# Optimization experiments

Measured on AMD Instinct MI355X. Metric: run time of the kernel, lower is better.

Reference implementation:

```python
import jax, jax.numpy as jnp
import numpy as np

N = 100000   # nodes
E = 300000   # directed edges (avg degree 3, molecular graphs)
G = 4000     # molecules in the batch
IN = 9
HID = 128
HEADS = 4
NEG_SLOPE = 0.2


def setup_inputs() -> dict:
    key = jax.random.key(0)
    ks = jax.random.split(key, 12)
    x = jax.random.normal(ks[0], (N, IN), dtype=jnp.float32)
    edge_index = jax.random.randint(ks[1], (2, E), 0, N, dtype=jnp.int32)
    batch = jnp.sort(jax.random.randint(ks[2], (N,), 0, G, dtype=jnp.int32))
    s = 0.1  # keep activations in a sane range
    W1 = jax.random.normal(ks[3], (IN, HEADS * HID), dtype=jnp.float32) * s
    a_src1 = jax.random.normal(ks[4], (HEADS, HID), dtype=jnp.float32) * s
    a_dst1 = jax.random.normal(ks[5], (HEADS, HID), dtype=jnp.float32) * s
    b1 = jax.random.normal(ks[6], (HEADS * HID,), dtype=jnp.float32) * s
    W2 = jax.random.normal(ks[7], (HEADS * HID, HID), dtype=jnp.float32) * s
    a_src2 = jax.random.normal(ks[8], (1, HID), dtype=jnp.float32) * s
    a_dst2 = jax.random.normal(ks[9], (1, HID), dtype=jnp.float32) * s
    b2 = jax.random.normal(ks[10], (HID,), dtype=jnp.float32) * s
    return {"x": x, "edge_index": edge_index, "batch": batch,
            "W1": W1, "a_src1": a_src1, "a_dst1": a_dst1, "b1": b1,
            "W2": W2, "a_src2": a_src2, "a_dst2": a_dst2, "b2": b2}


def _gat_conv(x, edge_index, W, a_src, a_dst, b, heads, out_ch, concat):
    """PyG GATConv: linear proj, per-edge leaky-relu attention logits,
    segment softmax over destination nodes, scatter-add aggregation.
    add_self_loops=True (PyG default)."""
    n = x.shape[0]
    loops = jnp.arange(n, dtype=edge_index.dtype)
    src = jnp.concatenate([edge_index[0], loops])
    dst = jnp.concatenate([edge_index[1], loops])

    h = (x @ W).reshape(n, heads, out_ch)                  # [N, H, C]
    alpha_s = jnp.einsum('nhc,hc->nh', h, a_src)           # [N, H]
    alpha_d = jnp.einsum('nhc,hc->nh', h, a_dst)           # [N, H]

    logits = jax.nn.leaky_relu(alpha_s[src] + alpha_d[dst], NEG_SLOPE)  # [Etot, H]
    # numerically stable segment softmax over incoming edges of each dst
    m = jax.ops.segment_max(logits, dst, num_segments=n)   # [N, H] (finite: self-loops)
    e = jnp.exp(logits - m[dst])
    z = jax.ops.segment_sum(e, dst, num_segments=n)
    alpha = e / (z[dst] + 1e-16)                           # [Etot, H]

    msg = h[src] * alpha[:, :, None]                       # [Etot, H, C]
    out = jax.ops.segment_sum(msg, dst, num_segments=n)    # [N, H, C]
    if concat:
        out = out.reshape(n, heads * out_ch)
    else:
        out = out.mean(axis=1)
    return out + b


def reference(x, edge_index, batch, W1, a_src1, a_dst1, b1, W2, a_src2, a_dst2, b2):
    h = jax.nn.elu(_gat_conv(x, edge_index, W1, a_src1, a_dst1, b1, HEADS, HID, True))
    h = jax.nn.elu(_gat_conv(h, edge_index, W2, a_src2, a_dst2, b2, 1, HID, True))
    # global mean pool per graph
    sums = jax.ops.segment_sum(h, batch, num_segments=G)   # [G, HID]
    cnt = jax.ops.segment_sum(jnp.ones((h.shape[0],), h.dtype), batch, num_segments=G)
    return sums / jnp.maximum(cnt, 1.0)[:, None]
```

## Files before the change

### kernel.cpp

```cpp
#include <hip/hip_runtime.h>

#define N_NODES 100000
#define N_EDGES 300000
#define N_GRAPHS 4000
#define CAP 32

typedef float f32x4 __attribute__((ext_vector_type(4)));
typedef __bf16 bf16x8 __attribute__((ext_vector_type(8)));
typedef __bf16 bf16x2 __attribute__((ext_vector_type(2)));

static const size_t OFF_XA    = 0;
static const size_t OFF_AD4   = OFF_XA + (size_t)N_NODES * 16;
static const size_t OFF_AGG   = OFF_AD4 + (size_t)N_NODES * 4;
static const size_t OFF_P2B   = OFF_AGG + (size_t)N_NODES * 36;
static const size_t OFF_ASAD2 = OFF_P2B + (size_t)N_NODES * 64;
static const size_t OFF_WSB   = OFF_ASAD2 + (size_t)N_NODES * 2;
static const size_t OFF_INVC  = OFF_WSB + 32768;
static const size_t OFF_INT   = OFF_INVC + 4096;

#define PRE_NODE_END 391
#define PRE_PACKB_END 455
#define PRE_DEG_END 846
#define PRE_OUT_END 1346
#define PRE_INV_END 1362

__device__ __forceinline__ float lrelu(float x) { return x < 0.f ? 0.2f * x : x; }
__device__ __forceinline__ float elu(float x)   { return x > 0.f ? x : __expf(x) - 1.f; }

__global__ __launch_bounds__(256) void k_pre(
    const float* __restrict__ x, const float* __restrict__ W1,
    const float* __restrict__ a_src1, const float* __restrict__ a_dst1,
    const float* __restrict__ W2, const int* __restrict__ batch,
    float* __restrict__ xa, float* __restrict__ ad4,
    __bf16* __restrict__ wsB, int* __restrict__ deg, float* __restrict__ out,
    float* __restrict__ inv_cnt) {
    int b = blockIdx.x, tid = threadIdx.x;
    if (b < PRE_NODE_END) {
        __shared__ float wf[72];
        if (tid < 72) {
            int isd = tid / 36, r = tid % 36, k = r / 4, h = r % 4;
            const float* a = isd ? a_dst1 : a_src1;
            float s = 0.f;
            for (int c = 0; c < 128; c++) s += W1[k * 512 + h * 128 + c] * a[h * 128 + c];
            wf[tid] = s;
        }
        __syncthreads();
        int n = b * 256 + tid;
        if (n >= N_NODES) return;
        float xv[9];
#pragma unroll
        for (int k = 0; k < 9; k++) xv[k] = x[n * 9 + k];
        float as[4], ad[4];
#pragma unroll
        for (int h = 0; h < 4; h++) {
            float s = 0.f, d = 0.f;
#pragma unroll
            for (int k = 0; k < 9; k++) {
                s += xv[k] * wf[k * 4 + h];
                d += xv[k] * wf[36 + k * 4 + h];
            }
            as[h] = s; ad[h] = d;
        }
        f32x4* xp = (f32x4*)(xa + (size_t)n * 16);
        xp[0] = (f32x4){xv[0], xv[1], xv[2], xv[3]};
        xp[1] = (f32x4){xv[4], xv[5], xv[6], xv[7]};
        xp[2] = (f32x4){xv[8], as[0], as[1], as[2]};
        xp[3] = (f32x4){as[3], 0.f, 0.f, 0.f};
        *(f32x4*)(ad4 + (size_t)n * 4) = (f32x4){ad[0], ad[1], ad[2], ad[3]};
    } else if (b < PRE_PACKB_END) {
        int t = (b - PRE_NODE_END) * 256 + tid;
#pragma unroll
        for (int m = 0; m < 4; m++) {
            int idx = t * 4 + m;
            int k = idx >> 7, nn = idx & 127;
            wsB[(size_t)nn * 512 + k] = (__bf16)W2[(size_t)k * 128 + nn];
        }
    } else if (b < PRE_DEG_END) {
        int idx = (b - PRE_PACKB_END) * 256 + tid;
        if (idx < N_NODES) deg[idx] = 0;
    } else if (b < PRE_OUT_END) {
        int idx = (b - PRE_DEG_END) * 256 + tid;
        if (idx < 128000) ((f32x4*)out)[idx] = (f32x4){0.f, 0.f, 0.f, 0.f};
    } else {
        int g = (b - PRE_OUT_END) * 256 + tid;
        if (g >= N_GRAPHS) return;
        int lo = 0, hi = N_NODES;
        while (lo < hi) { int mid = (lo + hi) >> 1; if (batch[mid] < g) lo = mid + 1; else hi = mid; }
        int s = lo; hi = N_NODES;
        while (lo < hi) { int mid = (lo + hi) >> 1; if (batch[mid] < g + 1) lo = mid + 1; else hi = mid; }
        int c = lo - s;
        inv_cnt[g] = 1.f / (float)(c > 0 ? c : 1);
    }
}

__global__ void k_bucket(const int* __restrict__ ei, int* __restrict__ deg,
                         int* __restrict__ bucket) {
    int e = blockIdx.x * 256 + threadIdx.x;
    if (e >= N_EDGES) return;
    int s = ei[e], d = ei[N_EDGES + e];
    int slot = atomicAdd(&deg[d], 1);
    if (slot < CAP) bucket[d * CAP + slot] = s;
}

__global__ void k_agg(const float* __restrict__ xa, const float* __restrict__ ad4,
                      const int* __restrict__ deg, const int* __restrict__ bucket,
                      __bf16* __restrict__ agg) {
    int t = blockIdx.x * 256 + threadIdx.x;
    int n = t >> 2, h = t & 3;
    if (n >= N_NODES) return;
    float ad = ad4[(size_t)n * 4 + h];
    int dg = deg[n];
    if (dg > CAP) dg = CAP;
    float acc[9] = {};
    float z = 0.f;
    {
        const f32x4* xp = (const f32x4*)(xa + (size_t)n * 16);
        f32x4 v0 = xp[0], v1 = xp[1], v2 = xp[2], v3 = xp[3];
        float asl = (h == 0) ? v2.y : (h == 1) ? v2.z : (h == 2) ? v2.w : v3.x;
        float e = __expf(lrelu(asl + ad));
        z += e;
        acc[0] += e * v0.x; acc[1] += e * v0.y; acc[2] += e * v0.z; acc[3] += e * v0.w;
        acc[4] += e * v1.x; acc[5] += e * v1.y; acc[6] += e * v1.z; acc[7] += e * v1.w;
        acc[8] += e * v2.x;
    }
    for (int j = 0; j < dg; j++) {
        int src = bucket[n * CAP + j];
        const f32x4* xp = (const f32x4*)(xa + (size_t)src * 16);
        f32x4 v0 = xp[0], v1 = xp[1], v2 = xp[2], v3 = xp[3];
        float asl = (h == 0) ? v2.y : (h == 1) ? v2.z : (h == 2) ? v2.w : v3.x;
        float e = __expf(lrelu(asl + ad));
        z += e;
        acc[0] += e * v0.x; acc[1] += e * v0.y; acc[2] += e * v0.z; acc[3] += e * v0.w;
        acc[4] += e * v1.x; acc[5] += e * v1.y; acc[6] += e * v1.z; acc[7] += e * v1.w;
        acc[8] += e * v2.x;
    }
    float inv = 1.f / z;
    bf16x8 p0;
#pragma unroll
    for (int k = 0; k < 8; k++) p0[k] = (__bf16)(acc[k] * inv);
    __bf16* dst = agg + (size_t)n * 72 + h * 16;
    *(bf16x8*)dst = p0;
    dst[8] = (__bf16)(acc[8] * inv);
}

__global__ __launch_bounds__(512, 4) void k_gemm(
    const __bf16* __restrict__ agg, const float* __restrict__ W1,
    const float* __restrict__ b1, const __bf16* __restrict__ wsB,
    const float* __restrict__ a_src2, const float* __restrict__ a_dst2,
    __bf16* __restrict__ p2b, float* __restrict__ asad2) {
    __shared__ __bf16 As[64 * 512];
    __shared__ __bf16 AgT[64 * 72];
    __shared__ float red2[64 * 16];
    const int tid = threadIdx.x;
    const int lane = tid & 63;
    const int w = tid >> 6;
    const int i = lane & 15;
    const int q = lane >> 4;
    const int m0 = blockIdx.x * 64;

    bf16x8 breg[16];
    {
        const __bf16* bp = wsB + (size_t)(w * 16 + i) * 512 + q * 8;
#pragma unroll
        for (int kc = 0; kc < 16; kc++) breg[kc] = *(const bf16x8*)(bp + kc * 32);
    }

    for (int idx = tid; idx < 576; idx += 512) {
        int row = idx / 9, c8 = idx - row * 9;
        int gr = m0 + row;
        bf16x8 v;
        if (gr < N_NODES) v = *(const bf16x8*)(agg + (size_t)gr * 72 + c8 * 8);
        else {
#pragma unroll
            for (int k = 0; k < 8; k++) v[k] = (__bf16)0.f;
        }
        *(bf16x8*)&AgT[row * 72 + c8 * 8] = v;
    }
    __syncthreads();

    {
        int row = tid & 63;
        int kg = __builtin_amdgcn_readfirstlane(tid >> 6);
        int h = kg >> 1;
        float ag[9];
        {
            bf16x8 a8 = *(const bf16x8*)&AgT[row * 72 + h * 16];
#pragma unroll
            for (int k = 0; k < 8; k++) ag[k] = (float)a8[k];
            ag[8] = (float)AgT[row * 72 + h * 16 + 8];
        }
        int rt = row >> 4, il = row & 15;
#pragma unroll
        for (int c8 = 0; c8 < 8; c8++) {
            int j0 = kg * 64 + c8 * 8;
            float o[8];
#pragma unroll
            for (int e = 0; e < 8; e++) o[e] = b1[j0 + e];
#pragma unroll
            for (int k = 0; k < 9; k++) {
                const float* wp = &W1[k * 512 + j0];
#pragma unroll
                for (int e = 0; e < 8; e++) o[e] += ag[k] * wp[e];
            }
            bf16x8 pk;
#pragma unroll
            for (int e = 0; e < 8; e++) pk[e] = (__bf16)elu(o[e]);
            int tile = rt * 16 + (kg * 2 + (c8 >> 2));
            *(bf16x8*)&As[tile * 512 + ((c8 & 3) * 16 + il) * 8] = pk;
        }
    }
    __syncthreads();

    f32x4 acc[4];
#pragma unroll
    for (int r = 0; r < 4; r++) acc[r] = (f32x4){0.f, 0.f, 0.f, 0.f};
#pragma unroll
    for (int kc = 0; kc < 16; kc++) {
#pragma unroll
        for (int rt = 0; rt < 4; rt++) {
            bf16x8 af = *(const bf16x8*)&As[(rt * 16 + kc) * 512 + lane * 8];
            acc[rt] = __builtin_amdgcn_mfma_f32_16x16x32_bf16(af, breg[kc], acc[rt], 0, 0, 0);
        }
    }

    float as2 = a_src2[w * 16 + i];
    float ad2 = a_dst2[w * 16 + i];
#pragma unroll
    for (int rt = 0; rt < 4; rt++) {
#pragma unroll
        for (int qq = 0; qq < 4; qq++) {
            int row = rt * 16 + q * 4 + qq;
            float v = acc[rt][qq];
            if (m0 + row < N_NODES)
                p2b[(size_t)(m0 + row) * 128 + w * 16 + i] = (__bf16)v;
            float s = v * as2, d = v * ad2;
#pragma unroll
            for (int off = 1; off < 16; off <<= 1) {
                s += __shfl_xor(s, off);
                d += __shfl_xor(d, off);
            }
            if (i == 0) {
                red2[row * 16 + w * 2] = s;
                red2[row * 16 + w * 2 + 1] = d;
            }
        }
    }
    __syncthreads();
    if (tid < 128) {
        int row = tid >> 1, cc = tid & 1;
        float sum = 0.f;
#pragma unroll
        for (int ww = 0; ww < 8; ww++) sum += red2[row * 16 + ww * 2 + cc];
        if (m0 + row < N_NODES) asad2[(size_t)(m0 + row) * 2 + cc] = sum;
    }
}

__global__ void k_agg2_pool(const __bf16* __restrict__ p2b, const float* __restrict__ asad2,
                            const int* __restrict__ deg, const int* __restrict__ bucket,
                            const float* __restrict__ b2, const int* __restrict__ batch,
                            const float* __restrict__ inv_cnt, float* __restrict__ out) {
    int wv = (blockIdx.x * 256 + threadIdx.x) >> 6;
    wv = __builtin_amdgcn_readfirstlane(wv);
    int lane = threadIdx.x & 63;
    int nbase = wv * 8;
    if (nbase >= N_NODES) return;
    int nend = nbase + 8;
    if (nend > N_NODES) nend = N_NODES;
    float b2a = b2[2 * lane], b2b = b2[2 * lane + 1];
    float g0 = 0.f, g1 = 0.f;
    int curg = batch[nbase];
    for (int n = nbase; n < nend; n++) {
        float ad = asad2[n * 2 + 1];
        float e = __expf(lrelu(asad2[n * 2] + ad));
        float z = e;
        bf16x2 v = ((const bf16x2*)(p2b + (size_t)n * 128))[lane];
        float a0 = e * (float)v.x;
        float a1 = e * (float)v.y;
        int dg = deg[n];
        if (dg > CAP) dg = CAP;
        for (int j = 0; j < dg; j++) {
            int s = bucket[n * CAP + j];
            float e2 = __expf(lrelu(asad2[s * 2] + ad));
            z += e2;
            bf16x2 sv = ((const bf16x2*)(p2b + (size_t)s * 128))[lane];
            a0 += e2 * (float)sv.x;
            a1 += e2 * (float)sv.y;
        }
        float inv = 1.f / z;
        float o0 = elu(a0 * inv + b2a);
        float o1 = elu(a1 * inv + b2b);
        int g = batch[n];
        if (g != curg) {
            float ic = inv_cnt[curg];
            atomicAdd(&out[(size_t)curg * 128 + 2 * lane], g0 * ic);
            atomicAdd(&out[(size_t)curg * 128 + 2 * lane + 1], g1 * ic);
            g0 = 0.f; g1 = 0.f; curg = g;
        }
        g0 += o0; g1 += o1;
    }
    float ic = inv_cnt[curg];
    atomicAdd(&out[(size_t)curg * 128 + 2 * lane], g0 * ic);
    atomicAdd(&out[(size_t)curg * 128 + 2 * lane + 1], g1 * ic);
}

extern "C" void kernel_launch(void* const* d_in, const int* in_sizes, int n_in,
                              void* d_out, int out_size, void* d_ws, size_t ws_size,
                              hipStream_t stream) {
    const float* x       = (const float*)d_in[0];
    const int*   ei      = (const int*)d_in[1];
    const int*   batch   = (const int*)d_in[2];
    const float* W1      = (const float*)d_in[3];
    const float* a_src1  = (const float*)d_in[4];
    const float* a_dst1  = (const float*)d_in[5];
    const float* b1      = (const float*)d_in[6];
    const float* W2      = (const float*)d_in[7];
    const float* a_src2  = (const float*)d_in[8];
    const float* a_dst2  = (const float*)d_in[9];
    const float* b2      = (const float*)d_in[10];
    float* out = (float*)d_out;

    float* wsf   = (float*)d_ws;
    float* xa    = wsf + OFF_XA;
    float* ad4   = wsf + OFF_AD4;
    __bf16* agg  = (__bf16*)(wsf + OFF_AGG);
    __bf16* p2b  = (__bf16*)(wsf + OFF_P2B);
    float* asad2 = wsf + OFF_ASAD2;
    __bf16* wsB  = (__bf16*)(wsf + OFF_WSB);
    float* invc  = wsf + OFF_INVC;
    int* wsi    = (int*)(wsf + OFF_INT);
    int* deg    = wsi;
    int* bucket = wsi + N_NODES;

    k_pre<<<PRE_INV_END, 256, 0, stream>>>(x, W1, a_src1, a_dst1, W2, batch,
                                           xa, ad4, wsB, deg, out, invc);
    k_bucket<<<(N_EDGES + 255) / 256, 256, 0, stream>>>(ei, deg, bucket);
    k_agg<<<(N_NODES * 4 + 255) / 256, 256, 0, stream>>>(xa, ad4, deg, bucket, agg);
    k_gemm<<<(N_NODES + 63) / 64, 512, 0, stream>>>(agg, W1, b1, wsB,
                                                    a_src2, a_dst2, p2b, asad2);
    k_agg2_pool<<<((N_NODES + 7) / 8 * 64 + 255) / 256, 256, 0, stream>>>(
        p2b, asad2, deg, bucket, b2, batch, invc, out);
}
```

Baseline: 224.6 us.

## Fuse layer-1 neighbor aggregation into GEMM kernel and halve its LDS tile

The layer-1 attention aggregation kernel is folded into the GEMM kernel. Each block now gathers its 64 nodes' neighbor features straight into shared memory, with two threads per (node, head) splitting the edges and combining results through a shuffle. This removes one launch and the bf16 agg round trip through global memory. The A tile is built and consumed in two K-halves, which halves LDS use and lets the launch bound rise to 6 blocks per CU. The cost is extra syncs, W1 projection work split per half, and B fragments reloaded per half.

```diff
diff --git a/kernel.cpp b/kernel.cpp
--- a/kernel.cpp
+++ b/kernel.cpp
@@ -11,8 +11,7 @@
 
 static const size_t OFF_XA    = 0;
 static const size_t OFF_AD4   = OFF_XA + (size_t)N_NODES * 16;
-static const size_t OFF_AGG   = OFF_AD4 + (size_t)N_NODES * 4;
-static const size_t OFF_P2B   = OFF_AGG + (size_t)N_NODES * 36;
+static const size_t OFF_P2B   = OFF_AD4 + (size_t)N_NODES * 4;
 static const size_t OFF_ASAD2 = OFF_P2B + (size_t)N_NODES * 64;
 static const size_t OFF_WSB   = OFF_ASAD2 + (size_t)N_NODES * 2;
 static const size_t OFF_INVC  = OFF_WSB + 32768;
@@ -102,53 +101,14 @@
     if (slot < CAP) bucket[d * CAP + slot] = s;
 }
 
-__global__ void k_agg(const float* __restrict__ xa, const float* __restrict__ ad4,
-                      const int* __restrict__ deg, const int* __restrict__ bucket,
-                      __bf16* __restrict__ agg) {
-    int t = blockIdx.x * 256 + threadIdx.x;
-    int n = t >> 2, h = t & 3;
-    if (n >= N_NODES) return;
-    float ad = ad4[(size_t)n * 4 + h];
-    int dg = deg[n];
-    if (dg > CAP) dg = CAP;
-    float acc[9] = {};
-    float z = 0.f;
-    {
-        const f32x4* xp = (const f32x4*)(xa + (size_t)n * 16);
-        f32x4 v0 = xp[0], v1 = xp[1], v2 = xp[2], v3 = xp[3];
-        float asl = (h == 0) ? v2.y : (h == 1) ? v2.z : (h == 2) ? v2.w : v3.x;
-        float e = __expf(lrelu(asl + ad));
-        z += e;
-        acc[0] += e * v0.x; acc[1] += e * v0.y; acc[2] += e * v0.z; acc[3] += e * v0.w;
-        acc[4] += e * v1.x; acc[5] += e * v1.y; acc[6] += e * v1.z; acc[7] += e * v1.w;
-        acc[8] += e * v2.x;
-    }
-    for (int j = 0; j < dg; j++) {
-        int src = bucket[n * CAP + j];
-        const f32x4* xp = (const f32x4*)(xa + (size_t)src * 16);
-        f32x4 v0 = xp[0], v1 = xp[1], v2 = xp[2], v3 = xp[3];
-        float asl = (h == 0) ? v2.y : (h == 1) ? v2.z : (h == 2) ? v2.w : v3.x;
-        float e = __expf(lrelu(asl + ad));
-        z += e;
-        acc[0] += e * v0.x; acc[1] += e * v0.y; acc[2] += e * v0.z; acc[3] += e * v0.w;
-        acc[4] += e * v1.x; acc[5] += e * v1.y; acc[6] += e * v1.z; acc[7] += e * v1.w;
-        acc[8] += e * v2.x;
-    }
-    float inv = 1.f / z;
-    bf16x8 p0;
-#pragma unroll
-    for (int k = 0; k < 8; k++) p0[k] = (__bf16)(acc[k] * inv);
-    __bf16* dst = agg + (size_t)n * 72 + h * 16;
-    *(bf16x8*)dst = p0;
-    dst[8] = (__bf16)(acc[8] * inv);
-}
-
-__global__ __launch_bounds__(512, 4) void k_gemm(
-    const __bf16* __restrict__ agg, const float* __restrict__ W1,
-    const float* __restrict__ b1, const __bf16* __restrict__ wsB,
+__global__ __launch_bounds__(512, 6) void k_gemm(
+    const float* __restrict__ xa, const float* __restrict__ ad4,
+    const int* __restrict__ deg, const int* __restrict__ bucket,
+    const float* __restrict__ W1, const float* __restrict__ b1,
+    const __bf16* __restrict__ wsB,
     const float* __restrict__ a_src2, const float* __restrict__ a_dst2,
     __bf16* __restrict__ p2b, float* __restrict__ asad2) {
-    __shared__ __bf16 As[64 * 512];
+    __shared__ __bf16 As[64 * 256];
     __shared__ __bf16 AgT[64 * 72];
     __shared__ float red2[64 * 16];
     const int tid = threadIdx.x;
@@ -158,69 +118,108 @@
     const int q = lane >> 4;
     const int m0 = blockIdx.x * 64;
 
-    bf16x8 breg[16];
     {
-        const __bf16* bp = wsB + (size_t)(w * 16 + i) * 512 + q * 8;
-#pragma unroll
-        for (int kc = 0; kc < 16; kc++) breg[kc] = *(const bf16x8*)(bp + kc * 32);
-    }
-
-    for (int idx = tid; idx < 576; idx += 512) {
-        int row = idx / 9, c8 = idx - row * 9;
-        int gr = m0 + row;
-        bf16x8 v;
-        if (gr < N_NODES) v = *(const bf16x8*)(agg + (size_t)gr * 72 + c8 * 8);
-        else {
-#pragma unroll
-            for (int k = 0; k < 8; k++) v[k] = (__bf16)0.f;
-        }
-        *(bf16x8*)&AgT[row * 72 + c8 * 8] = v;
+        int nh = tid >> 1, sub = tid & 1;
+        int r = nh >> 2, h = nh & 3;
+        int n = m0 + r;
+        float acc[9] = {};
+        float z = 0.f;
+        bool valid = (n < N_NODES);
+        if (valid) {
+            float ad = ad4[(size_t)n * 4 + h];
+            int dg = deg[n];
+            if (dg > CAP) dg = CAP;
+            if (sub == 0) {
+                const f32x4* xp = (const f32x4*)(xa + (size_t)n * 16);
+                f32x4 v0 = xp[0], v1 = xp[1], v2 = xp[2], v3 = xp[3];
+                float asl = (h == 0) ? v2.y : (h == 1) ? v2.z : (h == 2) ? v2.w : v3.x;
+                float e = __expf(lrelu(asl + ad));
+                z += e;
+                acc[0] += e * v0.x; acc[1] += e * v0.y; acc[2] += e * v0.z; acc[3] += e * v0.w;
+                acc[4] += e * v1.x; acc[5] += e * v1.y; acc[6] += e * v1.z; acc[7] += e * v1.w;
+                acc[8] += e * v2.x;
+            }
+            for (int j = sub; j < dg; j += 2) {
+                int src = bucket[n * CAP + j];
+                const f32x4* xp = (const f32x4*)(xa + (size_t)src * 16);
+                f32x4 v0 = xp[0], v1 = xp[1], v2 = xp[2], v3 = xp[3];
+                float asl = (h == 0) ? v2.y : (h == 1) ? v2.z : (h == 2) ? v2.w : v3.x;
+                float e = __expf(lrelu(asl + ad));
+                z += e;
+                acc[0] += e * v0.x; acc[1] += e * v0.y; acc[2] += e * v0.z; acc[3] += e * v0.w;
+                acc[4] += e * v1.x; acc[5] += e * v1.y; acc[6] += e * v1.z; acc[7] += e * v1.w;
+                acc[8] += e * v2.x;
+            }
+        }
+        z += __shfl_xor(z, 1);
+#pragma unroll
+        for (int k = 0; k < 9; k++) acc[k] += __shfl_xor(acc[k], 1);
+        if (sub == 0) {
+            float inv = valid ? 1.f / z : 0.f;
+            bf16x8 p0;
+#pragma unroll
+            for (int k = 0; k < 8; k++) p0[k] = (__bf16)(acc[k] * inv);
+            __bf16* dst = AgT + r * 72 + h * 16;
+            *(bf16x8*)dst = p0;
+            dst[8] = (__bf16)(acc[8] * inv);
+        }
     }
     __syncthreads();
 
-    {
-        int row = tid & 63;
-        int kg = __builtin_amdgcn_readfirstlane(tid >> 6);
-        int h = kg >> 1;
-        float ag[9];
+    f32x4 acc[4];
+#pragma unroll
+    for (int r = 0; r < 4; r++) acc[r] = (f32x4){0.f, 0.f, 0.f, 0.f};
+
+    const int row = tid & 63;
+    const int kg = __builtin_amdgcn_readfirstlane(tid >> 6);
+    const int rt_p1 = row >> 4, il = row & 15;
+    const __bf16* bcol = wsB + (size_t)(w * 16 + i) * 512 + q * 8;
+
+#pragma unroll
+    for (int half = 0; half < 2; half++) {
+        bf16x8 breg[8];
+#pragma unroll
+        for (int kc = 0; kc < 8; kc++)
+            breg[kc] = *(const bf16x8*)(bcol + half * 256 + kc * 32);
+
         {
-            bf16x8 a8 = *(const bf16x8*)&AgT[row * 72 + h * 16];
-#pragma unroll
-            for (int k = 0; k < 8; k++) ag[k] = (float)a8[k];
-            ag[8] = (float)AgT[row * 72 + h * 16 + 8];
-        }
-        int rt = row >> 4, il = row & 15;
-#pragma unroll
-        for (int c8 = 0; c8 < 8; c8++) {
-            int j0 = kg * 64 + c8 * 8;
-            float o[8];
-#pragma unroll
-            for (int e = 0; e < 8; e++) o[e] = b1[j0 + e];
-#pragma unroll
-            for (int k = 0; k < 9; k++) {
-                const float* wp = &W1[k * 512 + j0];
-#pragma unroll
-                for (int e = 0; e < 8; e++) o[e] += ag[k] * wp[e];
-            }
-            bf16x8 pk;
-#pragma unroll
-            for (int e = 0; e < 8; e++) pk[e] = (__bf16)elu(o[e]);
-            int tile = rt * 16 + (kg * 2 + (c8 >> 2));
-            *(bf16x8*)&As[tile * 512 + ((c8 & 3) * 16 + il) * 8] = pk;
-        }
-    }
-    __syncthreads();
-
-    f32x4 acc[4];
-#pragma unroll
-    for (int r = 0; r < 4; r++) acc[r] = (f32x4){0.f, 0.f, 0.f, 0.f};
-#pragma unroll
-    for (int kc = 0; kc < 16; kc++) {
-#pragma unroll
-        for (int rt = 0; rt < 4; rt++) {
-            bf16x8 af = *(const bf16x8*)&As[(rt * 16 + kc) * 512 + lane * 8];
-            acc[rt] = __builtin_amdgcn_mfma_f32_16x16x32_bf16(af, breg[kc], acc[rt], 0, 0, 0);
-        }
+            int h = half * 2 + (kg >> 2);
+            float ag[9];
+            {
+                bf16x8 a8 = *(const bf16x8*)&AgT[row * 72 + h * 16];
+#pragma unroll
+                for (int k = 0; k < 8; k++) ag[k] = (float)a8[k];
+                ag[8] = (float)AgT[row * 72 + h * 16 + 8];
+            }
+#pragma unroll
+            for (int c8 = 0; c8 < 4; c8++) {
+                int j0 = half * 256 + kg * 32 + c8 * 8;
+                float o[8];
+#pragma unroll
+                for (int e = 0; e < 8; e++) o[e] = b1[j0 + e];
+#pragma unroll
+                for (int k = 0; k < 9; k++) {
+                    const float* wp = &W1[k * 512 + j0];
+#pragma unroll
+                    for (int e = 0; e < 8; e++) o[e] += ag[k] * wp[e];
+                }
+                bf16x8 pk;
+#pragma unroll
+                for (int e = 0; e < 8; e++) pk[e] = (__bf16)elu(o[e]);
+                *(bf16x8*)&As[(rt_p1 * 8 + kg) * 512 + (c8 * 16 + il) * 8] = pk;
+            }
+        }
+        __syncthreads();
+
+#pragma unroll
+        for (int kc = 0; kc < 8; kc++) {
+#pragma unroll
+            for (int rt = 0; rt < 4; rt++) {
+                bf16x8 af = *(const bf16x8*)&As[(rt * 8 + kc) * 512 + lane * 8];
+                acc[rt] = __builtin_amdgcn_mfma_f32_16x16x32_bf16(af, breg[kc], acc[rt], 0, 0, 0);
+            }
+        }
+        __syncthreads();
     }
 
     float as2 = a_src2[w * 16 + i];
@@ -229,10 +228,10 @@
     for (int rt = 0; rt < 4; rt++) {
 #pragma unroll
         for (int qq = 0; qq < 4; qq++) {
-            int row = rt * 16 + q * 4 + qq;
+            int r2 = rt * 16 + q * 4 + qq;
             float v = acc[rt][qq];
-            if (m0 + row < N_NODES)
-                p2b[(size_t)(m0 + row) * 128 + w * 16 + i] = (__bf16)v;
+            if (m0 + r2 < N_NODES)
+                p2b[(size_t)(m0 + r2) * 128 + w * 16 + i] = (__bf16)v;
             float s = v * as2, d = v * ad2;
 #pragma unroll
             for (int off = 1; off < 16; off <<= 1) {
@@ -240,18 +239,18 @@
                 d += __shfl_xor(d, off);
             }
             if (i == 0) {
-                red2[row * 16 + w * 2] = s;
-                red2[row * 16 + w * 2 + 1] = d;
+                red2[r2 * 16 + w * 2] = s;
+                red2[r2 * 16 + w * 2 + 1] = d;
             }
         }
     }
     __syncthreads();
     if (tid < 128) {
-        int row = tid >> 1, cc = tid & 1;
+        int r2 = tid >> 1, cc = tid & 1;
         float sum = 0.f;
 #pragma unroll
-        for (int ww = 0; ww < 8; ww++) sum += red2[row * 16 + ww * 2 + cc];
-        if (m0 + row < N_NODES) asad2[(size_t)(m0 + row) * 2 + cc] = sum;
+        for (int ww = 0; ww < 8; ww++) sum += red2[r2 * 16 + ww * 2 + cc];
+        if (m0 + r2 < N_NODES) asad2[(size_t)(m0 + r2) * 2 + cc] = sum;
     }
 }
 
@@ -322,7 +321,6 @@
     float* wsf   = (float*)d_ws;
     float* xa    = wsf + OFF_XA;
     float* ad4   = wsf + OFF_AD4;
-    __bf16* agg  = (__bf16*)(wsf + OFF_AGG);
     __bf16* p2b  = (__bf16*)(wsf + OFF_P2B);
     float* asad2 = wsf + OFF_ASAD2;
     __bf16* wsB  = (__bf16*)(wsf + OFF_WSB);
@@ -334,9 +332,8 @@
     k_pre<<<PRE_INV_END, 256, 0, stream>>>(x, W1, a_src1, a_dst1, W2, batch,
                                            xa, ad4, wsB, deg, out, invc);
     k_bucket<<<(N_EDGES + 255) / 256, 256, 0, stream>>>(ei, deg, bucket);
-    k_agg<<<(N_NODES * 4 + 255) / 256, 256, 0, stream>>>(xa, ad4, deg, bucket, agg);
-    k_gemm<<<(N_NODES + 63) / 64, 512, 0, stream>>>(agg, W1, b1, wsB,
-                                                    a_src2, a_dst2, p2b, asad2);
+    k_gemm<<<(N_NODES + 63) / 64, 512, 0, stream>>>(xa, ad4, deg, bucket, W1, b1,
+                                                    wsB, a_src2, a_dst2, p2b, asad2);
     k_agg2_pool<<<((N_NODES + 7) / 8 * 64 + 255) / 256, 256, 0, stream>>>(
         p2b, asad2, deg, bucket, b2, batch, invc, out);
 }
```

After: 217.0 us. -3.4%, faster.
